# Kernel tuning notes

Measured on AMD Instinct MI355X. Metric: run time of the kernel, lower is better.

## Reference

```python
import jax, jax.numpy as jnp
import numpy as np


def setup_inputs() -> dict:
    key = jax.random.key(0)
    k_u, k_K, k_D = jax.random.split(key, 3)
    B, H, L = 8, 256, 8192
    u = jax.random.normal(k_u, (B, H, L), dtype=jnp.float32)
    # K: SSM convolution kernel buffer of shape (H, L) (output of VandermondeReservoir)
    K = jax.random.normal(k_K, (H, L), dtype=jnp.float32)
    # D: skip-connection scale, uniform in [min_scaleD, max_scaleD] = [0, 1]
    D = jax.random.uniform(k_D, (H,), dtype=jnp.float32, minval=0.0, maxval=1.0)
    return {"u": u, "K": K, "D": D}


def reference(u, K, D):
    """FFT-based long convolution + skip add.

    u: (B, H, L) real input
    K: (H, L) convolution kernel
    D: (H,) skip scale
    Returns complex64 output of shape (B, H, L), matching torch.fft.ifft output dtype.
    """
    L = u.shape[-1]
    N = 2 * L - 1  # zero-padded linear-convolution length
    u_s = jnp.fft.fft(u, n=N, axis=-1)          # (B, H, N) complex
    k_s = jnp.fft.fft(K, n=N, axis=-1)          # (H, N) complex
    y = jnp.fft.ifft(u_s * k_s[None], n=N, axis=-1)[..., :L]  # (B, H, L) complex
    y = y + (D[None, :, None] * u).astype(y.dtype)            # skip add D * u
    return y
```

## Files before the change

### kernel.cpp

```cpp
#include <hip/hip_runtime.h>


#define TILE 128
#define IGRP 16
#define SLOTS 17
#define BROW 136
#define SLOT_STRIDE (8 * BROW)
#define BS_SHORTS (SLOTS * SLOT_STRIDE)
#define KRC_STRIDE 264
#define KRC_BUF (8 * KRC_STRIDE)
#define EP_STRIDE 132

typedef short bf16x8 __attribute__((ext_vector_type(8)));
typedef float f32x4 __attribute__((ext_vector_type(4)));

__device__ __forceinline__ unsigned short f2bf(float f) {
    unsigned int u = __float_as_uint(f);
    u = (u + 0x7fffu + ((u >> 16) & 1u)) >> 16;
    return (unsigned short)u;
}

__global__ __launch_bounds__(256) void build_KR8(
    const float* __restrict__ K, unsigned short* __restrict__ KR8, int L, int RS) {
    int x0 = (blockIdx.x * 256 + threadIdx.x) * 4;
    int r = blockIdx.y;
    long h = blockIdx.z;
    if (x0 >= RS) return;
    const float* Kh = K + h * (long)L;
    unsigned short s[4];
    #pragma unroll
    for (int j = 0; j < 4; ++j) {
        int t = x0 + j - r;
        s[j] = (t >= 0 && t < L) ? f2bf(Kh[L - 1 - t]) : (unsigned short)0;
    }
    uint2 w;
    w.x = s[0] | ((unsigned)s[1] << 16);
    w.y = s[2] | ((unsigned)s[3] << 16);
    *(uint2*)(KR8 + (h * 8 + r) * (long)RS + x0) = w;
}

template <int UK>
__global__ __launch_bounds__(256, 3) void conv_main(
    const float* __restrict__ u, const float* __restrict__ Kc,
    const float* __restrict__ Dp, const unsigned short* __restrict__ KR8,
    float* __restrict__ outf, int H, int L, int G, int RS, int cplx, long out_floats)
{
    __shared__ __align__(16) char smem[UK ? (BS_SHORTS * 2) : (BS_SHORTS * 2 + 2 * KRC_BUF * 2)];
    unsigned short* Bs = (unsigned short*)smem;
    unsigned short* Krc = (unsigned short*)(smem + BS_SHORTS * 2);
    float* Ep = (float*)smem;

    const int tid  = threadIdx.x;
    const int lane = tid & 63;
    const int wv   = tid >> 6;
    const int wm   = wv >> 1;
    const int wn   = wv & 1;
    const int m    = lane & 15;
    const int quad = lane >> 4;
    const bool tb0 = (m < 8);

    const int bx = blockIdx.x;
    const int h  = bx % H;
    const int g  = (G - 1) - (bx / H);
    const int i0 = g * IGRP;
    const int dmax = i0 + IGRP - 1;

    const int rA = (m + 1) & 7;
    const int t0b = 127 - wm * 64 - m + quad * 8;
    const int cB = (m & 7) * BROW + quad * 8;

    const char* pA = (const char*)(KR8 + ((long)(h * 8 + rA)) * RS)
                   + 2 * ((long)(L - TILE) + t0b + rA);
    const int cAb = 2 * (rA * KRC_STRIDE + t0b + rA);

    int ldsK[5], taK[5];
    bool vK[5];
    if (UK == 0) {
        #pragma unroll
        for (int p = 0; p < 5; ++p) {
            int wi = tid + p * 256;
            vK[p] = wi < 1056;
            int rp = vK[p] ? (wi / 132) : 0;
            int tp = (wi - rp * 132) * 2;
            ldsK[p] = rp * KRC_STRIDE + tp;
            taK[p] = vK[p] ? (tp - rp) : -1000;
        }
    }
    const float* Kfrow = Kc + (long)h * L;

    const int bb = tid >> 5;
    const int q8 = (tid & 31) * 4;
    const long ubase = ((long)bb * H + h) * L;

    f32x4 acc[4][4];
    {
        f32x4 z = {0.f, 0.f, 0.f, 0.f};
        #pragma unroll
        for (int a = 0; a < 4; ++a)
            #pragma unroll
            for (int b = 0; b < 4; ++b) acc[a][b] = z;
    }

    int sc4[4];
    #pragma unroll
    for (int nb = 0; nb < 4; ++nb) {
        int il = wn * 8 + nb * 2 + (m >> 3);
        sc4[nb] = (i0 + il) % SLOTS;
    }
    int slotw = (i0 >= 1) ? ((i0 - 1) % SLOTS) : (SLOTS - 1);

    #pragma unroll
    for (int batch = 0; batch < 2; ++batch) {
        uint2 a8[8];
        #pragma unroll
        for (int q = 0; q < 8; ++q) {
            int j = i0 + batch * 8 + q;
            float4 v = *(const float4*)(u + ubase + (long)j * TILE + q8);
            a8[q].x = f2bf(v.x) | ((unsigned)f2bf(v.y) << 16);
            a8[q].y = f2bf(v.z) | ((unsigned)f2bf(v.w) << 16);
        }
        #pragma unroll
        for (int q = 0; q < 8; ++q) {
            int j = i0 + batch * 8 + q;
            *(uint2*)(Bs + (j % SLOTS) * SLOT_STRIDE + bb * BROW + q8) = a8[q];
        }
    }
    if (UK == 0) {
        #pragma unroll
        for (int p = 0; p < 5; ++p) {
            if (vK[p]) {
                unsigned int s0 = 0, s1 = 0;
                int ta = taK[p];
                int ka = 127 - ta;
                if (ta >= 0 && ta < 256 && ka >= 0) s0 = f2bf(Kfrow[ka]);
                if (ta + 1 >= 0 && ta + 1 < 256 && (ka - 1) >= 0) s1 = f2bf(Kfrow[ka - 1]);
                *(unsigned int*)(Krc + ldsK[p]) = s0 | (s1 << 16);
            }
        }
    }
    bf16x8 af[10], afn[5] = {};
    if (UK) {
        #pragma unroll
        for (int o = 0; o < 5; ++o) af[o] = *(const bf16x8*)(pA + (o - 3) * 32);
    }
    __syncthreads();

    const bf16x8 z8 = {};

    for (int d = 0; d <= dmax; ++d) {
        const int dn = d + 1;
        const int jn = i0 - 1 - d;

        if (UK) {
            #pragma unroll
            for (int o = 5; o < 10; ++o) af[o] = *(const bf16x8*)(pA + (o - 3) * 32);
        } else {
            const char* Ab = (const char*)Krc + (d & 1) * (KRC_BUF * 2) + cAb;
            #pragma unroll
            for (int o = 0; o < 10; ++o) af[o] = *(const bf16x8*)(Ab + (o - 3) * 32);
        }

        float4 fv = {0.f, 0.f, 0.f, 0.f};
        if (jn >= 0)
            fv = *(const float4*)(u + ubase + (long)jn * TILE + q8);

        if (UK) {
            if (d < dmax) {
                #pragma unroll
                for (int o = 0; o < 5; ++o) afn[o] = *(const bf16x8*)(pA - 256 + (o - 3) * 32);
            }
        }
        unsigned int kv[5] = {0u, 0u, 0u, 0u, 0u};
        if (UK == 0 && dn <= dmax) {
            #pragma unroll
            for (int p = 0; p < 5; ++p) {
                unsigned int s0 = 0, s1 = 0;
                int ta = taK[p];
                if (vK[p]) {
                    int ka = dn * TILE + 127 - ta;
                    if (ta >= 0 && ta < 256 && ka >= 0) s0 = f2bf(Kfrow[ka]);
                    if (ta + 1 >= 0 && ta + 1 < 256 && (ka - 1) >= 0) s1 = f2bf(Kfrow[ka - 1]);
                }
                kv[p] = s0 | (s1 << 16);
            }
        }

        const int dlim = d - i0;
        const unsigned short* Bp[4];
        #pragma unroll
        for (int nb = 0; nb < 4; ++nb)
            Bp[nb] = Bs + sc4[nb] * SLOT_STRIDE + cB;

        __builtin_amdgcn_s_setprio(1);
        #pragma unroll
        for (int kc = 0; kc < 4; ++kc) {
            #pragma unroll
            for (int nb = 0; nb < 4; ++nb) {
                const int nbg = wn * 4 + nb;
                if (2 * nbg + 1 >= dlim) {
                    bf16x8 bfr = *(const bf16x8*)(Bp[nb] + kc * 32);
                    if (2 * nbg + 1 == dlim) bfr = tb0 ? z8 : bfr;
                    acc[0][nb] = __builtin_amdgcn_mfma_f32_16x16x32_bf16(af[3 + 2 * kc], bfr, acc[0][nb], 0, 0, 0);
                    acc[1][nb] = __builtin_amdgcn_mfma_f32_16x16x32_bf16(af[2 + 2 * kc], bfr, acc[1][nb], 0, 0, 0);
                    acc[2][nb] = __builtin_amdgcn_mfma_f32_16x16x32_bf16(af[1 + 2 * kc], bfr, acc[2][nb], 0, 0, 0);
                    acc[3][nb] = __builtin_amdgcn_mfma_f32_16x16x32_bf16(af[0 + 2 * kc], bfr, acc[3][nb], 0, 0, 0);
                }
            }
        }
        __builtin_amdgcn_s_setprio(0);

        if (UK == 0 && dn <= dmax) {
            unsigned short* Kw = Krc + (dn & 1) * KRC_BUF;
            #pragma unroll
            for (int p = 0; p < 5; ++p)
                if (vK[p]) *(unsigned int*)(Kw + ldsK[p]) = kv[p];
        }
        if (jn >= 0) {
            uint2 bv;
            bv.x = f2bf(fv.x) | ((unsigned)f2bf(fv.y) << 16);
            bv.y = f2bf(fv.z) | ((unsigned)f2bf(fv.w) << 16);
            *(uint2*)(Bs + slotw * SLOT_STRIDE + bb * BROW + q8) = bv;
        }

        slotw = slotw ? slotw - 1 : SLOTS - 1;
        #pragma unroll
        for (int nb = 0; nb < 4; ++nb)
            sc4[nb] = sc4[nb] ? sc4[nb] - 1 : SLOTS - 1;
        if (UK) {
            #pragma unroll
            for (int o = 0; o < 5; ++o) af[o] = afn[o];
            pA -= 256;
        }
        __syncthreads();
    }

    const float Dh = Dp[h];
    const int ec = tid >> 2;
    const int ps = (tid & 3) * 32;
    #pragma unroll
    for (int pass = 0; pass < 2; ++pass) {
        if (wn == pass) {
            #pragma unroll
            for (int rb = 0; rb < 4; ++rb) {
                int p = wm * 64 + rb * 16 + quad * 4;
                #pragma unroll
                for (int nb = 0; nb < 4; ++nb) {
                    int cloc = nb * 16 + m;
                    *(f32x4*)(Ep + cloc * EP_STRIDE + p) = acc[rb][nb];
                }
            }
        }
        __syncthreads();
        {
            int cg = pass * 64 + ec;
            int b  = cg & 7;
            int i  = i0 + (cg >> 3);
            long base = ((long)b * H + h) * L + (long)i * TILE + ps;
            const float* ep = Ep + ec * EP_STRIDE + ps;
            const float* us = u + base;
            if (cplx) {
                if (2 * (base + 32) <= out_floats) {
                    float4* o = (float4*)(outf + 2 * base);
                    #pragma unroll
                    for (int k4 = 0; k4 < 8; ++k4) {
                        float4 uv = ((const float4*)us)[k4];
                        float4 ev = *(const float4*)(ep + k4 * 4);
                        float4 o1, o2;
                        o1.x = ev.x + Dh * uv.x; o1.y = 0.f;
                        o1.z = ev.y + Dh * uv.y; o1.w = 0.f;
                        o2.x = ev.z + Dh * uv.z; o2.y = 0.f;
                        o2.z = ev.w + Dh * uv.w; o2.w = 0.f;
                        o[k4 * 2]     = o1;
                        o[k4 * 2 + 1] = o2;
                    }
                }
            } else {
                if (base + 32 <= out_floats) {
                    float4* o = (float4*)(outf + base);
                    #pragma unroll
                    for (int k4 = 0; k4 < 8; ++k4) {
                        float4 uv = ((const float4*)us)[k4];
                        float4 ev = *(const float4*)(ep + k4 * 4);
                        float4 ov;
                        ov.x = ev.x + Dh * uv.x;
                        ov.y = ev.y + Dh * uv.y;
                        ov.z = ev.z + Dh * uv.z;
                        ov.w = ev.w + Dh * uv.w;
                        o[k4] = ov;
                    }
                }
            }
        }
        __syncthreads();
    }
}

extern "C" void kernel_launch(void* const* d_in, const int* in_sizes, int n_in,
                              void* d_out, int out_size, void* d_ws, size_t ws_size,
                              hipStream_t stream) {
    const float* u  = (const float*)d_in[0];
    const float* Kc = (const float*)d_in[1];
    const float* Dp = (const float*)d_in[2];
    const int H = in_sizes[2];
    const int L = in_sizes[1] / H;
    const int G = L / (TILE * IGRP);
    const int RS = L + 272;
    const int cplx = (out_size >= 2 * in_sizes[0]) ? 1 : 0;

    const size_t kr8_bytes = (size_t)H * 8 * RS * 2;
    const int tier = (ws_size >= kr8_bytes) ? 1 : 0;
    unsigned short* KR8 = (unsigned short*)d_ws;

    if (tier) {
        dim3 gk((RS / 4 + 255) / 256, 8, H);
        build_KR8<<<gk, 256, 0, stream>>>(Kc, KR8, L, RS);
        conv_main<1><<<H * G, 256, 0, stream>>>(u, Kc, Dp, KR8, (float*)d_out,
                                                H, L, G, RS, cplx, (long)out_size);
    } else {
        conv_main<0><<<H * G, 256, 0, stream>>>(u, Kc, Dp, KR8, (float*)d_out,
                                                H, L, G, RS, cplx, (long)out_size);
    }
}
```

Baseline: 293.9 us.

## Process two diagonal steps per barrier in UK path with deeper slot ring

In the precomputed-kernel (UK) path, the main loop is restructured so each iteration runs two diagonal compute steps between barriers. This halves the number of __syncthreads and batches the global loads of the next two u tiles. The LDS ring grows from 17 to 19 slots, and the prologue preloads one extra tile so the two writes per iteration cannot overwrite slots still being read. The per-step half-tile zero masking is removed and replaced by a zero-filled slot at j=-1. The added LDS use may reduce occupancy, and the changed masking and slot indexing carry correctness risk.

```diff
diff --git a/kernel.cpp b/kernel.cpp
--- a/kernel.cpp
+++ b/kernel.cpp
@@ -3,7 +3,7 @@
 
 #define TILE 128
 #define IGRP 16
-#define SLOTS 17
+#define SLOTS 19
 #define BROW 136
 #define SLOT_STRIDE (8 * BROW)
 #define BS_SHORTS (SLOTS * SLOT_STRIDE)
@@ -39,6 +39,34 @@
     *(uint2*)(KR8 + (h * 8 + r) * (long)RS + x0) = w;
 }
 
+#define COMPUTE_STEP(S_DLIM)                                                            \
+    {                                                                                   \
+        const int dlim = (S_DLIM);                                                      \
+        const unsigned short* Bp[4];                                                    \
+        _Pragma("unroll")                                                               \
+        for (int nb = 0; nb < 4; ++nb)                                                  \
+            Bp[nb] = Bs + sc4[nb] * SLOT_STRIDE + cB;                                   \
+        __builtin_amdgcn_s_setprio(1);                                                  \
+        _Pragma("unroll")                                                               \
+        for (int kc = 0; kc < 4; ++kc) {                                                \
+            _Pragma("unroll")                                                           \
+            for (int nb = 0; nb < 4; ++nb) {                                            \
+                const int nbg = wn * 4 + nb;                                            \
+                if (2 * nbg + 1 >= dlim) {                                              \
+                    bf16x8 bfr = *(const bf16x8*)(Bp[nb] + kc * 32);                    \
+                    acc[0][nb] = __builtin_amdgcn_mfma_f32_16x16x32_bf16(af[3 + 2*kc], bfr, acc[0][nb], 0, 0, 0); \
+                    acc[1][nb] = __builtin_amdgcn_mfma_f32_16x16x32_bf16(af[2 + 2*kc], bfr, acc[1][nb], 0, 0, 0); \
+                    acc[2][nb] = __builtin_amdgcn_mfma_f32_16x16x32_bf16(af[1 + 2*kc], bfr, acc[2][nb], 0, 0, 0); \
+                    acc[3][nb] = __builtin_amdgcn_mfma_f32_16x16x32_bf16(af[0 + 2*kc], bfr, acc[3][nb], 0, 0, 0); \
+                }                                                                       \
+            }                                                                           \
+        }                                                                               \
+        __builtin_amdgcn_s_setprio(0);                                                  \
+        _Pragma("unroll")                                                               \
+        for (int nb = 0; nb < 4; ++nb)                                                  \
+            sc4[nb] = sc4[nb] ? sc4[nb] - 1 : SLOTS - 1;                                \
+    }
+
 template <int UK>
 __global__ __launch_bounds__(256, 3) void conv_main(
     const float* __restrict__ u, const float* __restrict__ Kc,
@@ -57,7 +85,6 @@
     const int wn   = wv & 1;
     const int m    = lane & 15;
     const int quad = lane >> 4;
-    const bool tb0 = (m < 8);
 
     const int bx = blockIdx.x;
     const int h  = bx % H;
@@ -107,22 +134,30 @@
         int il = wn * 8 + nb * 2 + (m >> 3);
         sc4[nb] = (i0 + il) % SLOTS;
     }
-    int slotw = (i0 >= 1) ? ((i0 - 1) % SLOTS) : (SLOTS - 1);
-
-    #pragma unroll
-    for (int batch = 0; batch < 2; ++batch) {
-        uint2 a8[8];
-        #pragma unroll
-        for (int q = 0; q < 8; ++q) {
-            int j = i0 + batch * 8 + q;
-            float4 v = *(const float4*)(u + ubase + (long)j * TILE + q8);
-            a8[q].x = f2bf(v.x) | ((unsigned)f2bf(v.y) << 16);
-            a8[q].y = f2bf(v.z) | ((unsigned)f2bf(v.w) << 16);
-        }
-        #pragma unroll
-        for (int q = 0; q < 8; ++q) {
-            int j = i0 + batch * 8 + q;
-            *(uint2*)(Bs + (j % SLOTS) * SLOT_STRIDE + bb * BROW + q8) = a8[q];
+
+    {
+        #pragma unroll
+        for (int batch = 0; batch < 2; ++batch) {
+            const int bn = batch ? 9 : 8;
+            uint2 a8[9];
+            #pragma unroll
+            for (int q = 0; q < 9; ++q) {
+                if (q < bn) {
+                    int j = i0 - 1 + batch * 8 + q;
+                    float4 v = {0.f, 0.f, 0.f, 0.f};
+                    if (j >= 0) v = *(const float4*)(u + ubase + (long)j * TILE + q8);
+                    a8[q].x = f2bf(v.x) | ((unsigned)f2bf(v.y) << 16);
+                    a8[q].y = f2bf(v.z) | ((unsigned)f2bf(v.w) << 16);
+                }
+            }
+            #pragma unroll
+            for (int q = 0; q < 9; ++q) {
+                if (q < bn) {
+                    int j = i0 - 1 + batch * 8 + q;
+                    int sl = (j >= 0) ? (j % SLOTS) : (SLOTS - 1);
+                    *(uint2*)(Bs + sl * SLOT_STRIDE + bb * BROW + q8) = a8[q];
+                }
+            }
         }
     }
     if (UK == 0) {
@@ -145,93 +180,129 @@
     }
     __syncthreads();
 
-    const bf16x8 z8 = {};
-
-    for (int d = 0; d <= dmax; ++d) {
-        const int dn = d + 1;
-        const int jn = i0 - 1 - d;
-
-        if (UK) {
+    if (UK) {
+        int slotw1 = (i0 - 2 + SLOTS) % SLOTS;
+        int slotw2 = (i0 - 3 + SLOTS) % SLOTS;
+        const int R = (i0 + IGRP) / 2;
+        for (int r = 0; r < R; ++r) {
+            const int d = 2 * r;
             #pragma unroll
             for (int o = 5; o < 10; ++o) af[o] = *(const bf16x8*)(pA + (o - 3) * 32);
-        } else {
-            const char* Ab = (const char*)Krc + (d & 1) * (KRC_BUF * 2) + cAb;
-            #pragma unroll
-            for (int o = 0; o < 10; ++o) af[o] = *(const bf16x8*)(Ab + (o - 3) * 32);
-        }
-
-        float4 fv = {0.f, 0.f, 0.f, 0.f};
-        if (jn >= 0)
-            fv = *(const float4*)(u + ubase + (long)jn * TILE + q8);
-
-        if (UK) {
-            if (d < dmax) {
-                #pragma unroll
-                for (int o = 0; o < 5; ++o) afn[o] = *(const bf16x8*)(pA - 256 + (o - 3) * 32);
-            }
-        }
-        unsigned int kv[5] = {0u, 0u, 0u, 0u, 0u};
-        if (UK == 0 && dn <= dmax) {
-            #pragma unroll
-            for (int p = 0; p < 5; ++p) {
-                unsigned int s0 = 0, s1 = 0;
-                int ta = taK[p];
-                if (vK[p]) {
-                    int ka = dn * TILE + 127 - ta;
-                    if (ta >= 0 && ta < 256 && ka >= 0) s0 = f2bf(Kfrow[ka]);
-                    if (ta + 1 >= 0 && ta + 1 < 256 && (ka - 1) >= 0) s1 = f2bf(Kfrow[ka - 1]);
-                }
-                kv[p] = s0 | (s1 << 16);
-            }
-        }
-
-        const int dlim = d - i0;
-        const unsigned short* Bp[4];
-        #pragma unroll
-        for (int nb = 0; nb < 4; ++nb)
-            Bp[nb] = Bs + sc4[nb] * SLOT_STRIDE + cB;
-
-        __builtin_amdgcn_s_setprio(1);
-        #pragma unroll
-        for (int kc = 0; kc < 4; ++kc) {
-            #pragma unroll
-            for (int nb = 0; nb < 4; ++nb) {
-                const int nbg = wn * 4 + nb;
-                if (2 * nbg + 1 >= dlim) {
-                    bf16x8 bfr = *(const bf16x8*)(Bp[nb] + kc * 32);
-                    if (2 * nbg + 1 == dlim) bfr = tb0 ? z8 : bfr;
-                    acc[0][nb] = __builtin_amdgcn_mfma_f32_16x16x32_bf16(af[3 + 2 * kc], bfr, acc[0][nb], 0, 0, 0);
-                    acc[1][nb] = __builtin_amdgcn_mfma_f32_16x16x32_bf16(af[2 + 2 * kc], bfr, acc[1][nb], 0, 0, 0);
-                    acc[2][nb] = __builtin_amdgcn_mfma_f32_16x16x32_bf16(af[1 + 2 * kc], bfr, acc[2][nb], 0, 0, 0);
-                    acc[3][nb] = __builtin_amdgcn_mfma_f32_16x16x32_bf16(af[0 + 2 * kc], bfr, acc[3][nb], 0, 0, 0);
-                }
-            }
-        }
-        __builtin_amdgcn_s_setprio(0);
-
-        if (UK == 0 && dn <= dmax) {
-            unsigned short* Kw = Krc + (dn & 1) * KRC_BUF;
-            #pragma unroll
-            for (int p = 0; p < 5; ++p)
-                if (vK[p]) *(unsigned int*)(Kw + ldsK[p]) = kv[p];
-        }
-        if (jn >= 0) {
-            uint2 bv;
-            bv.x = f2bf(fv.x) | ((unsigned)f2bf(fv.y) << 16);
-            bv.y = f2bf(fv.z) | ((unsigned)f2bf(fv.w) << 16);
-            *(uint2*)(Bs + slotw * SLOT_STRIDE + bb * BROW + q8) = bv;
-        }
-
-        slotw = slotw ? slotw - 1 : SLOTS - 1;
-        #pragma unroll
-        for (int nb = 0; nb < 4; ++nb)
-            sc4[nb] = sc4[nb] ? sc4[nb] - 1 : SLOTS - 1;
-        if (UK) {
+            #pragma unroll
+            for (int o = 0; o < 5; ++o) afn[o] = *(const bf16x8*)(pA - 256 + (o - 3) * 32);
+            const int t1 = i0 - d - 2, t2 = t1 - 1;
+            float4 fv1 = {0.f, 0.f, 0.f, 0.f}, fv2 = {0.f, 0.f, 0.f, 0.f};
+            if (t1 >= 0) fv1 = *(const float4*)(u + ubase + (long)t1 * TILE + q8);
+            if (t2 >= 0) fv2 = *(const float4*)(u + ubase + (long)t2 * TILE + q8);
+
+            COMPUTE_STEP(d - i0);
+
             #pragma unroll
             for (int o = 0; o < 5; ++o) af[o] = afn[o];
             pA -= 256;
-        }
-        __syncthreads();
+            #pragma unroll
+            for (int o = 5; o < 10; ++o) af[o] = *(const bf16x8*)(pA + (o - 3) * 32);
+            if (r + 1 < R) {
+                #pragma unroll
+                for (int o = 0; o < 5; ++o) afn[o] = *(const bf16x8*)(pA - 256 + (o - 3) * 32);
+            }
+
+            COMPUTE_STEP(d + 1 - i0);
+
+            #pragma unroll
+            for (int o = 0; o < 5; ++o) af[o] = afn[o];
+            pA -= 256;
+
+            if (t1 >= 0) {
+                uint2 bv;
+                bv.x = f2bf(fv1.x) | ((unsigned)f2bf(fv1.y) << 16);
+                bv.y = f2bf(fv1.z) | ((unsigned)f2bf(fv1.w) << 16);
+                *(uint2*)(Bs + slotw1 * SLOT_STRIDE + bb * BROW + q8) = bv;
+            }
+            if (t2 >= -1) {
+                uint2 bv;
+                bv.x = f2bf(fv2.x) | ((unsigned)f2bf(fv2.y) << 16);
+                bv.y = f2bf(fv2.z) | ((unsigned)f2bf(fv2.w) << 16);
+                *(uint2*)(Bs + slotw2 * SLOT_STRIDE + bb * BROW + q8) = bv;
+            }
+            slotw1 = (slotw1 >= 2) ? slotw1 - 2 : slotw1 + (SLOTS - 2);
+            slotw2 = (slotw2 >= 2) ? slotw2 - 2 : slotw2 + (SLOTS - 2);
+            __syncthreads();
+        }
+    } else {
+        const bool tb0 = (m < 8);
+        const bf16x8 z8 = {};
+        int slotw = (i0 >= 1) ? ((i0 - 1) % SLOTS) : (SLOTS - 1);
+        for (int d = 0; d <= dmax; ++d) {
+            const int dn = d + 1;
+            const int jn = i0 - 1 - d;
+
+            const char* Ab = (const char*)Krc + (d & 1) * (KRC_BUF * 2) + cAb;
+            #pragma unroll
+            for (int o = 0; o < 10; ++o) af[o] = *(const bf16x8*)(Ab + (o - 3) * 32);
+
+            float4 fv = {0.f, 0.f, 0.f, 0.f};
+            if (jn >= 0)
+                fv = *(const float4*)(u + ubase + (long)jn * TILE + q8);
+
+            unsigned int kv[5] = {0u, 0u, 0u, 0u, 0u};
+            if (dn <= dmax) {
+                #pragma unroll
+                for (int p = 0; p < 5; ++p) {
+                    unsigned int s0 = 0, s1 = 0;
+                    int ta = taK[p];
+                    if (vK[p]) {
+                        int ka = dn * TILE + 127 - ta;
+                        if (ta >= 0 && ta < 256 && ka >= 0) s0 = f2bf(Kfrow[ka]);
+                        if (ta + 1 >= 0 && ta + 1 < 256 && (ka - 1) >= 0) s1 = f2bf(Kfrow[ka - 1]);
+                    }
+                    kv[p] = s0 | (s1 << 16);
+                }
+            }
+
+            const int dlim = d - i0;
+            const unsigned short* Bp[4];
+            #pragma unroll
+            for (int nb = 0; nb < 4; ++nb)
+                Bp[nb] = Bs + sc4[nb] * SLOT_STRIDE + cB;
+
+            __builtin_amdgcn_s_setprio(1);
+            #pragma unroll
+            for (int kc = 0; kc < 4; ++kc) {
+                #pragma unroll
+                for (int nb = 0; nb < 4; ++nb) {
+                    const int nbg = wn * 4 + nb;
+                    if (2 * nbg + 1 >= dlim) {
+                        bf16x8 bfr = *(const bf16x8*)(Bp[nb] + kc * 32);
+                        if (2 * nbg + 1 == dlim) bfr = tb0 ? z8 : bfr;
+                        acc[0][nb] = __builtin_amdgcn_mfma_f32_16x16x32_bf16(af[3 + 2 * kc], bfr, acc[0][nb], 0, 0, 0);
+                        acc[1][nb] = __builtin_amdgcn_mfma_f32_16x16x32_bf16(af[2 + 2 * kc], bfr, acc[1][nb], 0, 0, 0);
+                        acc[2][nb] = __builtin_amdgcn_mfma_f32_16x16x32_bf16(af[1 + 2 * kc], bfr, acc[2][nb], 0, 0, 0);
+                        acc[3][nb] = __builtin_amdgcn_mfma_f32_16x16x32_bf16(af[0 + 2 * kc], bfr, acc[3][nb], 0, 0, 0);
+                    }
+                }
+            }
+            __builtin_amdgcn_s_setprio(0);
+
+            if (dn <= dmax) {
+                unsigned short* Kw = Krc + (dn & 1) * KRC_BUF;
+                #pragma unroll
+                for (int p = 0; p < 5; ++p)
+                    if (vK[p]) *(unsigned int*)(Kw + ldsK[p]) = kv[p];
+            }
+            if (jn >= 0) {
+                uint2 bv;
+                bv.x = f2bf(fv.x) | ((unsigned)f2bf(fv.y) << 16);
+                bv.y = f2bf(fv.z) | ((unsigned)f2bf(fv.w) << 16);
+                *(uint2*)(Bs + slotw * SLOT_STRIDE + bb * BROW + q8) = bv;
+            }
+
+            slotw = slotw ? slotw - 1 : SLOTS - 1;
+            #pragma unroll
+            for (int nb = 0; nb < 4; ++nb)
+                sc4[nb] = sc4[nb] ? sc4[nb] - 1 : SLOTS - 1;
+            __syncthreads();
+        }
     }
 
     const float Dh = Dp[h];
```

Measured after the change: 295.0 us. About the same (+0.4%).

## Drop global Toeplitz kernel prebuild and stage K through LDS instead

Applied to the files above, without the earlier changes.

Removes the separate build_KR8 pass, which wrote eight shifted bf16 copies of K to workspace, and always uses the path that converts K into a double-buffered LDS tile each step. The slot ring grows from 17 to 19, and the prologue preloads one extra u tile (i0-1). This saves a kernel launch and the workspace write/read traffic. In exchange, every block redoes the K conversion and reads K from LDS, and the larger shared footprint may reduce occupancy.

```diff
diff --git a/kernel.cpp b/kernel.cpp
--- a/kernel.cpp
+++ b/kernel.cpp
@@ -3,7 +3,7 @@
 
 #define TILE 128
 #define IGRP 16
-#define SLOTS 17
+#define SLOTS 19
 #define BROW 136
 #define SLOT_STRIDE (8 * BROW)
 #define BS_SHORTS (SLOTS * SLOT_STRIDE)
@@ -20,32 +20,13 @@
     return (unsigned short)u;
 }
 
-__global__ __launch_bounds__(256) void build_KR8(
-    const float* __restrict__ K, unsigned short* __restrict__ KR8, int L, int RS) {
-    int x0 = (blockIdx.x * 256 + threadIdx.x) * 4;
-    int r = blockIdx.y;
-    long h = blockIdx.z;
-    if (x0 >= RS) return;
-    const float* Kh = K + h * (long)L;
-    unsigned short s[4];
-    #pragma unroll
-    for (int j = 0; j < 4; ++j) {
-        int t = x0 + j - r;
-        s[j] = (t >= 0 && t < L) ? f2bf(Kh[L - 1 - t]) : (unsigned short)0;
-    }
-    uint2 w;
-    w.x = s[0] | ((unsigned)s[1] << 16);
-    w.y = s[2] | ((unsigned)s[3] << 16);
-    *(uint2*)(KR8 + (h * 8 + r) * (long)RS + x0) = w;
-}
-
 template <int UK>
 __global__ __launch_bounds__(256, 3) void conv_main(
     const float* __restrict__ u, const float* __restrict__ Kc,
-    const float* __restrict__ Dp, const unsigned short* __restrict__ KR8,
-    float* __restrict__ outf, int H, int L, int G, int RS, int cplx, long out_floats)
+    const float* __restrict__ Dp,
+    float* __restrict__ outf, int H, int L, int G, int cplx, long out_floats)
 {
-    __shared__ __align__(16) char smem[UK ? (BS_SHORTS * 2) : (BS_SHORTS * 2 + 2 * KRC_BUF * 2)];
+    __shared__ __align__(16) char smem[BS_SHORTS * 2 + 2 * KRC_BUF * 2];
     unsigned short* Bs = (unsigned short*)smem;
     unsigned short* Krc = (unsigned short*)(smem + BS_SHORTS * 2);
     float* Ep = (float*)smem;
@@ -57,7 +38,6 @@
     const int wn   = wv & 1;
     const int m    = lane & 15;
     const int quad = lane >> 4;
-    const bool tb0 = (m < 8);
 
     const int bx = blockIdx.x;
     const int h  = bx % H;
@@ -69,13 +49,11 @@
     const int t0b = 127 - wm * 64 - m + quad * 8;
     const int cB = (m & 7) * BROW + quad * 8;
 
-    const char* pA = (const char*)(KR8 + ((long)(h * 8 + rA)) * RS)
-                   + 2 * ((long)(L - TILE) + t0b + rA);
     const int cAb = 2 * (rA * KRC_STRIDE + t0b + rA);
 
     int ldsK[5], taK[5];
     bool vK[5];
-    if (UK == 0) {
+    {
         #pragma unroll
         for (int p = 0; p < 5; ++p) {
             int wi = tid + p * 256;
@@ -107,25 +85,33 @@
         int il = wn * 8 + nb * 2 + (m >> 3);
         sc4[nb] = (i0 + il) % SLOTS;
     }
-    int slotw = (i0 >= 1) ? ((i0 - 1) % SLOTS) : (SLOTS - 1);
-
-    #pragma unroll
-    for (int batch = 0; batch < 2; ++batch) {
-        uint2 a8[8];
-        #pragma unroll
-        for (int q = 0; q < 8; ++q) {
-            int j = i0 + batch * 8 + q;
-            float4 v = *(const float4*)(u + ubase + (long)j * TILE + q8);
-            a8[q].x = f2bf(v.x) | ((unsigned)f2bf(v.y) << 16);
-            a8[q].y = f2bf(v.z) | ((unsigned)f2bf(v.w) << 16);
-        }
-        #pragma unroll
-        for (int q = 0; q < 8; ++q) {
-            int j = i0 + batch * 8 + q;
-            *(uint2*)(Bs + (j % SLOTS) * SLOT_STRIDE + bb * BROW + q8) = a8[q];
-        }
-    }
-    if (UK == 0) {
+
+    {
+        #pragma unroll
+        for (int batch = 0; batch < 2; ++batch) {
+            const int bn = batch ? 9 : 8;
+            uint2 a8[9];
+            #pragma unroll
+            for (int q = 0; q < 9; ++q) {
+                if (q < bn) {
+                    int j = i0 - 1 + batch * 8 + q;
+                    float4 v = {0.f, 0.f, 0.f, 0.f};
+                    if (j >= 0) v = *(const float4*)(u + ubase + (long)j * TILE + q8);
+                    a8[q].x = f2bf(v.x) | ((unsigned)f2bf(v.y) << 16);
+                    a8[q].y = f2bf(v.z) | ((unsigned)f2bf(v.w) << 16);
+                }
+            }
+            #pragma unroll
+            for (int q = 0; q < 9; ++q) {
+                if (q < bn) {
+                    int j = i0 - 1 + batch * 8 + q;
+                    int sl = (j >= 0) ? (j % SLOTS) : (SLOTS - 1);
+                    *(uint2*)(Bs + sl * SLOT_STRIDE + bb * BROW + q8) = a8[q];
+                }
+            }
+        }
+    }
+    {
         #pragma unroll
         for (int p = 0; p < 5; ++p) {
             if (vK[p]) {
@@ -138,40 +124,27 @@
             }
         }
     }
-    bf16x8 af[10], afn[5] = {};
-    if (UK) {
-        #pragma unroll
-        for (int o = 0; o < 5; ++o) af[o] = *(const bf16x8*)(pA + (o - 3) * 32);
-    }
+    bf16x8 af[10];
     __syncthreads();
 
+    const bool tb0 = (m < 8);
     const bf16x8 z8 = {};
 
+    int slotw = (i0 >= 1) ? ((i0 - 1) % SLOTS) : (SLOTS - 1);
     for (int d = 0; d <= dmax; ++d) {
         const int dn = d + 1;
         const int jn = i0 - 1 - d;
 
-        if (UK) {
-            #pragma unroll
-            for (int o = 5; o < 10; ++o) af[o] = *(const bf16x8*)(pA + (o - 3) * 32);
-        } else {
-            const char* Ab = (const char*)Krc + (d & 1) * (KRC_BUF * 2) + cAb;
-            #pragma unroll
-            for (int o = 0; o < 10; ++o) af[o] = *(const bf16x8*)(Ab + (o - 3) * 32);
-        }
+        const char* Ab = (const char*)Krc + (d & 1) * (KRC_BUF * 2) + cAb;
+        #pragma unroll
+        for (int o = 0; o < 10; ++o) af[o] = *(const bf16x8*)(Ab + (o - 3) * 32);
 
         float4 fv = {0.f, 0.f, 0.f, 0.f};
         if (jn >= 0)
             fv = *(const float4*)(u + ubase + (long)jn * TILE + q8);
 
-        if (UK) {
-            if (d < dmax) {
-                #pragma unroll
-                for (int o = 0; o < 5; ++o) afn[o] = *(const bf16x8*)(pA - 256 + (o - 3) * 32);
-            }
-        }
         unsigned int kv[5] = {0u, 0u, 0u, 0u, 0u};
-        if (UK == 0 && dn <= dmax) {
+        if (dn <= dmax) {
             #pragma unroll
             for (int p = 0; p < 5; ++p) {
                 unsigned int s0 = 0, s1 = 0;
@@ -209,7 +182,7 @@
         }
         __builtin_amdgcn_s_setprio(0);
 
-        if (UK == 0 && dn <= dmax) {
+        if (dn <= dmax) {
             unsigned short* Kw = Krc + (dn & 1) * KRC_BUF;
             #pragma unroll
             for (int p = 0; p < 5; ++p)
@@ -226,11 +199,6 @@
         #pragma unroll
         for (int nb = 0; nb < 4; ++nb)
             sc4[nb] = sc4[nb] ? sc4[nb] - 1 : SLOTS - 1;
-        if (UK) {
-            #pragma unroll
-            for (int o = 0; o < 5; ++o) af[o] = afn[o];
-            pA -= 256;
-        }
         __syncthreads();
     }
 
@@ -304,20 +272,8 @@
     const int H = in_sizes[2];
     const int L = in_sizes[1] / H;
     const int G = L / (TILE * IGRP);
-    const int RS = L + 272;
     const int cplx = (out_size >= 2 * in_sizes[0]) ? 1 : 0;
 
-    const size_t kr8_bytes = (size_t)H * 8 * RS * 2;
-    const int tier = (ws_size >= kr8_bytes) ? 1 : 0;
-    unsigned short* KR8 = (unsigned short*)d_ws;
-
-    if (tier) {
-        dim3 gk((RS / 4 + 255) / 256, 8, H);
-        build_KR8<<<gk, 256, 0, stream>>>(Kc, KR8, L, RS);
-        conv_main<1><<<H * G, 256, 0, stream>>>(u, Kc, Dp, KR8, (float*)d_out,
-                                                H, L, G, RS, cplx, (long)out_size);
-    } else {
-        conv_main<0><<<H * G, 256, 0, stream>>>(u, Kc, Dp, KR8, (float*)d_out,
-                                                H, L, G, RS, cplx, (long)out_size);
-    }
+    conv_main<0><<<H * G, 256, 0, stream>>>(u, Kc, Dp, (float*)d_out,
+                                            H, L, G, cplx, (long)out_size);
 }
```

Result: slower. 309.0 us (+5.1%).
